# Kernel optimization log

Measured on AMD Instinct MI355X. Metric: run time of the kernel, lower is better.

The kernel has to match this reference:

```python
import jax, jax.numpy as jnp
import numpy as np

N = 100000
E = 1600000
IN_C, HID_C, OUT_C = 64, 64, 32


def setup_inputs() -> dict:
    key = jax.random.key(0)
    ks = jax.random.split(key, 8)
    x = jax.random.normal(ks[0], (N, IN_C), dtype=jnp.float32)
    edge_index = jax.random.randint(ks[1], (2, E), 0, N, dtype=jnp.int64)
    # GCNConv weights (glorot-ish scale) and biases
    W1 = jax.random.normal(ks[2], (IN_C, HID_C), dtype=jnp.float32) / np.sqrt(IN_C)
    b1 = jnp.zeros((HID_C,), dtype=jnp.float32)
    W2 = jax.random.normal(ks[3], (HID_C, HID_C), dtype=jnp.float32) / np.sqrt(HID_C)
    b2 = jnp.zeros((HID_C,), dtype=jnp.float32)
    Wlin = jax.random.normal(ks[4], (HID_C, OUT_C), dtype=jnp.float32) / np.sqrt(HID_C)
    blin = jnp.zeros((OUT_C,), dtype=jnp.float32)
    return {"x": x, "edge_index": edge_index, "W1": W1, "b1": b1,
            "W2": W2, "b2": b2, "Wlin": Wlin, "blin": blin}


def _gcn_norm(edge_index):
    # PyG GCNConv default: add self-loops, symmetric normalization.
    loop = jnp.arange(N, dtype=edge_index.dtype)
    row = jnp.concatenate([edge_index[0], loop])  # source nodes [E+N]
    col = jnp.concatenate([edge_index[1], loop])  # target nodes [E+N]
    deg = jax.ops.segment_sum(jnp.ones_like(col, dtype=jnp.float32), col,
                              num_segments=N)
    dinv = jnp.where(deg > 0, deg ** -0.5, 0.0)
    norm = dinv[row] * dinv[col]  # [E+N]
    return row, col, norm


def _gcn_conv(h, W, b, row, col, norm):
    h = h @ W                                  # [N, F_out]
    msg = h[row] * norm[:, None]               # gather + scale, [E+N, F_out]
    out = jax.ops.segment_sum(msg, col, num_segments=N)  # scatter-add
    return out + b


def reference(x, edge_index, W1, b1, W2, b2, Wlin, blin):
    row, col, norm = _gcn_norm(edge_index)
    h = jax.nn.relu(_gcn_conv(x, W1, b1, row, col, norm))
    h = jax.nn.relu(_gcn_conv(h, W2, b2, row, col, norm))
    return h @ Wlin + blin
```

## Files before the change

### kernel.cpp

```cpp
#include <hip/hip_runtime.h>
#include <hip/hip_fp16.h>

#define IN_C 64
#define HID_C 64
#define OUT_C 32
#define S_NODES  512
#define S_CAP  12288
#define CHUNK_E 4096

typedef _Float16 f16_t;
typedef f16_t f16x2 __attribute__((ext_vector_type(2)));

__device__ __forceinline__ float dot2(unsigned int a, unsigned int b, float c) {
#if __has_builtin(__builtin_amdgcn_fdot2)
    return __builtin_amdgcn_fdot2(*(f16x2*)&a, *(f16x2*)&b, c, false);
#else
    float2 af = __half22float2(*(__half2*)&a);
    float2 bf = __half22float2(*(__half2*)&b);
    return fmaf(af.x, bf.x, fmaf(af.y, bf.y, c));
#endif
}

__device__ __forceinline__ int wave_iscan(int x, int lane) {
#pragma unroll
    for (int o = 1; o < 64; o <<= 1) {
        int y = __shfl_up(x, o);
        if (lane >= o) x += y;
    }
    return x;
}

__global__ __launch_bounds__(256) void fat(const void* ei, int E,
                                           int* bcur, int NB,
                                           int* __restrict__ staging,
                                           int NEB, int GB,
                                           const float* __restrict__ x,
                                           const float* __restrict__ W1,
                                           float* __restrict__ t32, int n,
                                           const float* __restrict__ W2,
                                           const float* __restrict__ Wlin,
                                           unsigned short* __restrict__ Wh2,
                                           unsigned short* __restrict__ Whl) {
    __shared__ __align__(16) int smem[5128];
    int tid = threadIdx.x;
    int b = blockIdx.x;
    if (b < NEB) {
        int* cnt = smem;          int* boff = smem + 256;
        int* lcur = smem + 512;   int* gbase = smem + 768;
        int* stg = smem + 1024;
        int* ps64 = smem + 5120;
        int* wsum = smem + 5121;
        int lane = tid & 63, wv = tid >> 6;
        if (tid == 0) *ps64 = 1;
        cnt[tid] = 0;
        __syncthreads();
        if (2 * tid + 1 < 2 * E && ((const int*)ei)[2 * tid + 1] != 0) *ps64 = 0;
        __syncthreads();
        int is64 = *ps64;
        int e0 = b * CHUNK_E;
        int e1 = min(E, e0 + CHUNK_E);
        const int* ei32 = (const int*)ei;
        int rbuf[16];
        int bbuf[16];
        if (is64) {
#pragma unroll
            for (int k = 0; k < 16; k++) {
                int e = e0 + (k << 8) + tid;
                if (e < e1) {
                    int src = ei32[2 * e];
                    int dst = ei32[2 * (E + e)];
                    rbuf[k] = src | ((dst & 511) << 17);
                    int bk = dst >> 9;
                    bbuf[k] = bk;
                    atomicAdd(&cnt[bk], 1);
                } else bbuf[k] = -1;
            }
        } else {
#pragma unroll
            for (int k = 0; k < 16; k++) {
                int e = e0 + (k << 8) + tid;
                if (e < e1) {
                    int src = ei32[e];
                    int dst = ei32[E + e];
                    rbuf[k] = src | ((dst & 511) << 17);
                    int bk = dst >> 9;
                    bbuf[k] = bk;
                    atomicAdd(&cnt[bk], 1);
                } else bbuf[k] = -1;
            }
        }
        __syncthreads();
        int v = cnt[tid];
        int xx = wave_iscan(v, lane);
        if (lane == 63) wsum[wv] = xx;
        __syncthreads();
        int add = 0;
#pragma unroll
        for (int w = 0; w < 3; w++) add += (w < wv) ? wsum[w] : 0;
        int bo = xx + add - v;
        boff[tid] = bo;
        lcur[tid] = bo;
        __syncthreads();
#pragma unroll
        for (int k = 0; k < 16; k++) {
            if (bbuf[k] >= 0) {
                int p = atomicAdd(&lcur[bbuf[k]], 1);
                stg[p] = rbuf[k];
            }
        }
        __syncthreads();
        if (tid < NB && cnt[tid] > 0) gbase[tid] = atomicAdd(&bcur[tid], cnt[tid]);
        __syncthreads();
        int sw = tid >> 4, sl = tid & 15;
        for (int bk = sw; bk < NB; bk += 16) {
            int c = cnt[bk];
            if (c == 0) continue;
            int o = boff[bk], g = gbase[bk];
            size_t gb = (size_t)bk * S_CAP;
            for (int j = sl; j < c; j += 16) {
                if (g + j < S_CAP) staging[gb + g + j] = stg[o + j];
            }
        }
    } else if (b < NEB + GB) {
        uint4* sA = (uint4*)smem;
        int bb = b - NEB;
        int lane = tid & 63, wave = tid >> 6;
        unsigned int wu[32];
#pragma unroll
        for (int k = 0; k < 32; k++) {
            f16x2 p;
            p.x = (f16_t)W1[(2 * k) * 64 + lane];
            p.y = (f16_t)W1[(2 * k + 1) * 64 + lane];
            wu[k] = *(unsigned int*)&p;
        }
        int base = bb * 32;
        const float2* A2 = (const float2*)x;
        int lim = n * 32;
        for (int i = tid; i < 1024; i += 256) {
            int gi = base * 32 + i;
            float2 v = (gi < lim) ? A2[gi] : make_float2(0.f, 0.f);
            ((__half2*)sA)[i] = __floats2half2_rn(v.x, v.y);
        }
        __syncthreads();
        int r0 = base + wave * 8;
        int r1 = min(r0 + 8, n);
        for (int r = r0; r < r1; r++) {
            int rr = r - base;
            float a0 = 0.f, a1 = 0.f;
#pragma unroll
            for (int j = 0; j < 8; j++) {
                uint4 u = sA[rr * 8 + j];
                a0 = dot2(u.x, wu[4 * j], a0);
                a1 = dot2(u.y, wu[4 * j + 1], a1);
                a0 = dot2(u.z, wu[4 * j + 2], a0);
                a1 = dot2(u.w, wu[4 * j + 3], a1);
            }
            t32[(size_t)r * 64 + lane] = a0 + a1;
        }
    } else {
        for (int i = tid; i < 4096; i += 256) {
            int r = i >> 6, c = i & 63;
            f16_t h2 = (f16_t)W2[r * 64 + c];
            Wh2[c * 64 + r] = *(unsigned short*)&h2;
        }
        for (int i = tid; i < 2048; i += 256) {
            int r = i >> 5, c = i & 31;
            f16_t h = (f16_t)Wlin[r * 32 + c];
            Whl[c * 64 + r] = *(unsigned short*)&h;
        }
    }
}

__global__ __launch_bounds__(256) void place_fine(const int* __restrict__ staging,
                                                  const int* __restrict__ bcur,
                                                  int* __restrict__ offs,
                                                  float* __restrict__ dinv,
                                                  int* __restrict__ rec,
                                                  const float* __restrict__ t32,
                                                  unsigned short* __restrict__ t16,
                                                  int N, int NB) {
    __shared__ int sdeg[S_NODES];
    __shared__ int curs[S_NODES];
    __shared__ int sb[256];
    __shared__ float sdinv[S_NODES];
    __shared__ int wsum[4];
    int tid = threadIdx.x;
    int lane = tid & 63, wv = tid >> 6;
    int v = (tid < NB) ? min(bcur[tid], S_CAP) : 0;
    sdeg[tid] = 0;
    sdeg[tid + 256] = 0;
    int xx = wave_iscan(v, lane);
    if (lane == 63) wsum[wv] = xx;
    __syncthreads();
    int add = 0;
#pragma unroll
    for (int w = 0; w < 3; w++) add += (w < wv) ? wsum[w] : 0;
    sb[tid] = xx + add;
    __syncthreads();
    int cnt = min(bcur[blockIdx.x], S_CAP);
    int bbase = sb[blockIdx.x] - cnt;
    if (blockIdx.x == NB - 1 && tid == 0) offs[N] = sb[255];
    int base = blockIdx.x * S_NODES;
    int nn = min(S_NODES, N - base);
    size_t sbase = (size_t)blockIdx.x * S_CAP;
    for (int j = tid; j < cnt; j += 256) atomicAdd(&sdeg[staging[sbase + j] >> 17], 1);
    __syncthreads();
    int d0 = sdeg[2 * tid], d1 = sdeg[2 * tid + 1];
    int t = d0 + d1;
    int x2 = wave_iscan(t, lane);
    if (lane == 63) wsum[wv] = x2;
    __syncthreads();
    int add2 = 0;
#pragma unroll
    for (int w = 0; w < 3; w++) add2 += (w < wv) ? wsum[w] : 0;
    int pre = bbase + x2 + add2 - t;
    curs[2 * tid] = pre;
    curs[2 * tid + 1] = pre + d0;
    float dv0 = rsqrtf((float)(d0 + 1));
    float dv1 = rsqrtf((float)(d1 + 1));
    sdinv[2 * tid] = dv0;
    sdinv[2 * tid + 1] = dv1;
    if (2 * tid < nn) {
        offs[base + 2 * tid] = pre;
        dinv[base + 2 * tid] = dv0;
    }
    if (2 * tid + 1 < nn) {
        offs[base + 2 * tid + 1] = pre + d0;
        dinv[base + 2 * tid + 1] = dv1;
    }
    __syncthreads();
    for (int j = tid; j < cnt; j += 256) {
        int pk = staging[sbase + j];
        int p = atomicAdd(&curs[pk >> 17], 1);
        rec[p] = pk & 0x1FFFF;
    }
    const float4* tin = (const float4*)t32 + (size_t)base * 16;
    uint2* tout = (uint2*)t16 + (size_t)base * 16;
    int jmax = nn * 16;
    for (int j = tid; j < jmax; j += 256) {
        float4 vv = tin[j];
        float w = sdinv[j >> 4];
        __half2 h0 = __floats2half2_rn(vv.x * w, vv.y * w);
        __half2 h1 = __floats2half2_rn(vv.z * w, vv.w * w);
        tout[j] = make_uint2(*(unsigned int*)&h0, *(unsigned int*)&h1);
    }
}

__device__ __forceinline__ void agg_consume(const uint4& v, float w, float s[8]) {
    float2 f0 = __half22float2(*(__half2*)&v.x);
    float2 f1 = __half22float2(*(__half2*)&v.y);
    float2 f2 = __half22float2(*(__half2*)&v.z);
    float2 f3 = __half22float2(*(__half2*)&v.w);
    s[0] = fmaf(f0.x, w, s[0]);
    s[1] = fmaf(f0.y, w, s[1]);
    s[2] = fmaf(f1.x, w, s[2]);
    s[3] = fmaf(f1.y, w, s[3]);
    s[4] = fmaf(f2.x, w, s[4]);
    s[5] = fmaf(f2.y, w, s[5]);
    s[6] = fmaf(f3.x, w, s[6]);
    s[7] = fmaf(f3.y, w, s[7]);
}

template <int NU>
__device__ __forceinline__ void agg_chunk(const uint4* __restrict__ t4,
                                          const int* __restrict__ rec,
                                          int beg, int node, int m, int i,
                                          int g, int gl, float s[8]) {
    int srcs[NU];
    float ws[NU];
    uint4 vs[NU];
#pragma unroll
    for (int u = 0; u < NU; u++) {
        int it = i + u * 8 + g;
        srcs[u] = (it == 0) ? node : ((it < m) ? rec[beg + it - 1] : node);
        ws[u] = (it < m) ? 1.f : 0.f;
    }
#pragma unroll
    for (int u = 0; u < NU; u++) vs[u] = t4[(size_t)srcs[u] * 8 + gl];
#pragma unroll
    for (int u = 0; u < NU; u++) agg_consume(vs[u], ws[u], s);
}

__global__ void aggregate(const unsigned short* __restrict__ t,
                          const int* __restrict__ offs, const int* __restrict__ rec,
                          const float* __restrict__ dinv, const float* __restrict__ bias,
                          unsigned short* __restrict__ acc, int n) {
    int wave = (blockIdx.x * blockDim.x + threadIdx.x) >> 6;
    int lane = threadIdx.x & 63;
    if (wave >= n) return;
    int g = lane >> 3;
    int gl = lane & 7;
    int beg = offs[wave], end = offs[wave + 1];
    int m = end - beg + 1;
    const uint4* t4 = (const uint4*)t;
    float s[8] = {0.f, 0.f, 0.f, 0.f, 0.f, 0.f, 0.f, 0.f};
    int i = 0;
    for (; m - i > 24; i += 32) agg_chunk<4>(t4, rec, beg, wave, m, i, g, gl, s);
    int rem = m - i;
    if (rem > 16)     agg_chunk<3>(t4, rec, beg, wave, m, i, g, gl, s);
    else if (rem > 8) agg_chunk<2>(t4, rec, beg, wave, m, i, g, gl, s);
    else if (rem > 0) agg_chunk<1>(t4, rec, beg, wave, m, i, g, gl, s);
#pragma unroll
    for (int k = 0; k < 8; k++) {
        s[k] += __shfl_xor(s[k], 8);
        s[k] += __shfl_xor(s[k], 16);
        s[k] += __shfl_xor(s[k], 32);
    }
    if (g == 0) {
        float d = dinv[wave];
        const float4* b4 = (const float4*)bias;
        float4 bb0 = b4[gl * 2], bb1 = b4[gl * 2 + 1];
        float o0 = fmaxf(fmaf(s[0], d, bb0.x), 0.f);
        float o1 = fmaxf(fmaf(s[1], d, bb0.y), 0.f);
        float o2 = fmaxf(fmaf(s[2], d, bb0.z), 0.f);
        float o3 = fmaxf(fmaf(s[3], d, bb0.w), 0.f);
        float o4 = fmaxf(fmaf(s[4], d, bb1.x), 0.f);
        float o5 = fmaxf(fmaf(s[5], d, bb1.y), 0.f);
        float o6 = fmaxf(fmaf(s[6], d, bb1.z), 0.f);
        float o7 = fmaxf(fmaf(s[7], d, bb1.w), 0.f);
        __half2 p0 = __floats2half2_rn(o0, o1);
        __half2 p1 = __floats2half2_rn(o2, o3);
        __half2 p2 = __floats2half2_rn(o4, o5);
        __half2 p3 = __floats2half2_rn(o6, o7);
        ((uint4*)acc)[(size_t)wave * 8 + gl] =
            make_uint4(*(unsigned int*)&p0, *(unsigned int*)&p1,
                       *(unsigned int*)&p2, *(unsigned int*)&p3);
    }
}

__global__ __launch_bounds__(256) void gemm64(const unsigned short* __restrict__ in,
                                              const unsigned short* __restrict__ Wh,
                                              unsigned short* __restrict__ out,
                                              const float* __restrict__ dinv, int n) {
    __shared__ uint4 sA[32 * 8];
    int tid = threadIdx.x;
    int lane = tid & 63, wave = tid >> 6;
    unsigned int wu[32];
    {
        const uint4* col = (const uint4*)(Wh + (size_t)lane * 64);
#pragma unroll
        for (int j = 0; j < 8; j++) {
            uint4 w4 = col[j];
            wu[4 * j] = w4.x; wu[4 * j + 1] = w4.y;
            wu[4 * j + 2] = w4.z; wu[4 * j + 3] = w4.w;
        }
    }
    int base = blockIdx.x * 32;
    const uint2* A2 = (const uint2*)in;
    int lim = n * 16;
    for (int i = tid; i < 512; i += 256) {
        int gi = base * 16 + i;
        ((uint2*)sA)[i] = (gi < lim) ? A2[gi] : make_uint2(0u, 0u);
    }
    __syncthreads();
    int r0 = base + wave * 8;
    int r1 = min(r0 + 8, n);
    for (int r = r0; r < r1; r++) {
        int rr = r - base;
        float a0 = 0.f, a1 = 0.f;
#pragma unroll
        for (int j = 0; j < 8; j++) {
            uint4 u = sA[rr * 8 + j];
            a0 = dot2(u.x, wu[4 * j], a0);
            a1 = dot2(u.y, wu[4 * j + 1], a1);
            a0 = dot2(u.z, wu[4 * j + 2], a0);
            a1 = dot2(u.w, wu[4 * j + 3], a1);
        }
        __half hv = __float2half_rn((a0 + a1) * dinv[r]);
        out[(size_t)r * 64 + lane] = *(unsigned short*)&hv;
    }
}

__global__ __launch_bounds__(256) void gemm32(const unsigned short* __restrict__ in,
                                              const unsigned short* __restrict__ Wh,
                                              const float* __restrict__ b,
                                              float* __restrict__ out, int n) {
    __shared__ uint4 sA[32 * 8];
    int tid = threadIdx.x;
    int lane = tid & 63, wave = tid >> 6;
    int c = lane & 31;
    unsigned int wu[32];
    {
        const uint4* col = (const uint4*)(Wh + (size_t)c * 64);
#pragma unroll
        for (int j = 0; j < 8; j++) {
            uint4 w4 = col[j];
            wu[4 * j] = w4.x; wu[4 * j + 1] = w4.y;
            wu[4 * j + 2] = w4.z; wu[4 * j + 3] = w4.w;
        }
    }
    float bl = b[c];
    int base = blockIdx.x * 32;
    const uint2* A2 = (const uint2*)in;
    int lim = n * 16;
    for (int i = tid; i < 512; i += 256) {
        int gi = base * 16 + i;
        ((uint2*)sA)[i] = (gi < lim) ? A2[gi] : make_uint2(0u, 0u);
    }
    __syncthreads();
    int r0 = base + wave * 8;
    int r1 = min(r0 + 8, n);
    for (int r = r0; r < r1; r++) {
        int rr = r - base;
        float a0 = 0.f, a1 = 0.f;
#pragma unroll
        for (int j = 0; j < 8; j++) {
            uint4 u = sA[rr * 8 + j];
            a0 = dot2(u.x, wu[4 * j], a0);
            a1 = dot2(u.y, wu[4 * j + 1], a1);
            a0 = dot2(u.z, wu[4 * j + 2], a0);
            a1 = dot2(u.w, wu[4 * j + 3], a1);
        }
        if (lane < 32) out[(size_t)r * 32 + c] = bl + a0 + a1;
    }
}

extern "C" void kernel_launch(void* const* d_in, const int* in_sizes, int n_in,
                              void* d_out, int out_size, void* d_ws, size_t ws_size,
                              hipStream_t stream) {
    (void)n_in; (void)out_size; (void)ws_size;
    const float* x    = (const float*)d_in[0];
    const void*  ei   = d_in[1];
    const float* W1   = (const float*)d_in[2];
    const float* b1   = (const float*)d_in[3];
    const float* W2   = (const float*)d_in[4];
    const float* b2   = (const float*)d_in[5];
    const float* Wlin = (const float*)d_in[6];
    const float* blin = (const float*)d_in[7];
    float* out = (float*)d_out;

    const int N = in_sizes[0] / IN_C;
    const int E = in_sizes[1] / 2;
    const int NB = (N + S_NODES - 1) / S_NODES;
    const int NEB = (E + CHUNK_E - 1) / CHUNK_E;
    const int GB = (N + 31) / 32;

    char* ws = (char*)d_ws;
    size_t off = 0;
    auto alloc = [&](size_t bytes) -> void* {
        size_t a = (off + 255) & ~(size_t)255;
        off = a + bytes;
        return (void*)(ws + a);
    };
    int*   offs    = (int*)  alloc((size_t)(N + 1) * 4);
    float* dinv    = (float*)alloc((size_t)N * 4);
    int*   bcur    = (int*)  alloc((size_t)NB * 4);
    int*   rec     = (int*)  alloc((size_t)E * 4);
    int*   staging = (int*)  alloc((size_t)NB * S_CAP * 4);
    float* t32     = (float*)alloc((size_t)N * HID_C * 4);
    unsigned short* t16 = (unsigned short*)alloc((size_t)N * HID_C * 2);
    unsigned short* Wh2 = (unsigned short*)alloc(64 * 64 * 2);
    unsigned short* Whl = (unsigned short*)alloc(64 * 32 * 2);
    unsigned short* acc = (unsigned short*)t32;

    hipMemsetAsync(bcur, 0, (size_t)NB * 4, stream);

    fat<<<NEB + GB + 1, 256, 0, stream>>>(ei, E, bcur, NB, staging, NEB, GB,
                                          x, W1, t32, N, W2, Wlin, Wh2, Whl);
    place_fine<<<NB, 256, 0, stream>>>(staging, bcur, offs, dinv, rec,
                                       t32, t16, N, NB);

    aggregate<<<(N + 3) / 4, 256, 0, stream>>>(t16, offs, rec, dinv, b1, acc, N);
    gemm64<<<GB, 256, 0, stream>>>(acc, Wh2, t16, dinv, N);
    aggregate<<<(N + 3) / 4, 256, 0, stream>>>(t16, offs, rec, dinv, b2, acc, N);
    gemm32<<<GB, 256, 0, stream>>>(acc, Whl, blin, out, N);
}
```

Baseline: 259.3 us.

## Widen place_fine to 1024 threads and use fma_mix in aggregation

The place_fine kernel now runs 1024 threads per block instead of 256. Each thread handles one node for the degree scan, and the loops over staging entries and feature conversion are strided by 1024, which gives more parallelism per block because there are only NB blocks. Separately, the aggregation inner loop replaces the half-to-float conversion plus FMA with inline v_fma_mix_f32 assembly, which multiplies an fp16 half directly into an fp32 accumulator. The inline asm ties the code to the CDNA ISA and may limit compiler scheduling.

```diff
diff --git a/kernel.cpp b/kernel.cpp
--- a/kernel.cpp
+++ b/kernel.cpp
@@ -19,6 +19,13 @@
     float2 bf = __half22float2(*(__half2*)&b);
     return fmaf(af.x, bf.x, fmaf(af.y, bf.y, c));
 #endif
+}
+
+__device__ __forceinline__ void mix2(float& s0, float& s1, unsigned int p, float w) {
+    asm("v_fma_mix_f32 %0, %2, %3, %0 op_sel:[0,0,0] op_sel_hi:[1,0,0]\n\t"
+        "v_fma_mix_f32 %1, %2, %3, %1 op_sel:[1,0,0] op_sel_hi:[1,0,0]"
+        : "+v"(s0), "+v"(s1)
+        : "v"(p), "v"(w));
 }
 
 __device__ __forceinline__ int wave_iscan(int x, int lane) {
@@ -171,31 +178,35 @@
     }
 }
 
-__global__ __launch_bounds__(256) void place_fine(const int* __restrict__ staging,
-                                                  const int* __restrict__ bcur,
-                                                  int* __restrict__ offs,
-                                                  float* __restrict__ dinv,
-                                                  int* __restrict__ rec,
-                                                  const float* __restrict__ t32,
-                                                  unsigned short* __restrict__ t16,
-                                                  int N, int NB) {
+__global__ __launch_bounds__(1024) void place_fine(const int* __restrict__ staging,
+                                                   const int* __restrict__ bcur,
+                                                   int* __restrict__ offs,
+                                                   float* __restrict__ dinv,
+                                                   int* __restrict__ rec,
+                                                   const float* __restrict__ t32,
+                                                   unsigned short* __restrict__ t16,
+                                                   int N, int NB) {
     __shared__ int sdeg[S_NODES];
     __shared__ int curs[S_NODES];
     __shared__ int sb[256];
     __shared__ float sdinv[S_NODES];
-    __shared__ int wsum[4];
+    __shared__ int wsum[16];
     int tid = threadIdx.x;
     int lane = tid & 63, wv = tid >> 6;
-    int v = (tid < NB) ? min(bcur[tid], S_CAP) : 0;
-    sdeg[tid] = 0;
-    sdeg[tid + 256] = 0;
-    int xx = wave_iscan(v, lane);
-    if (lane == 63) wsum[wv] = xx;
-    __syncthreads();
-    int add = 0;
-#pragma unroll
-    for (int w = 0; w < 3; w++) add += (w < wv) ? wsum[w] : 0;
-    sb[tid] = xx + add;
+    if (tid < S_NODES) sdeg[tid] = 0;
+    if (tid < 256) {
+        int v = (tid < NB) ? min(bcur[tid], S_CAP) : 0;
+        int xx = wave_iscan(v, lane);
+        if (lane == 63) wsum[wv] = xx;
+        sb[tid] = xx;
+    }
+    __syncthreads();
+    if (tid < 256) {
+        int add = 0;
+#pragma unroll
+        for (int w = 0; w < 3; w++) add += (w < wv) ? wsum[w] : 0;
+        sb[tid] += add;
+    }
     __syncthreads();
     int cnt = min(bcur[blockIdx.x], S_CAP);
     int bbase = sb[blockIdx.x] - cnt;
@@ -203,33 +214,27 @@
     int base = blockIdx.x * S_NODES;
     int nn = min(S_NODES, N - base);
     size_t sbase = (size_t)blockIdx.x * S_CAP;
-    for (int j = tid; j < cnt; j += 256) atomicAdd(&sdeg[staging[sbase + j] >> 17], 1);
-    __syncthreads();
-    int d0 = sdeg[2 * tid], d1 = sdeg[2 * tid + 1];
-    int t = d0 + d1;
-    int x2 = wave_iscan(t, lane);
-    if (lane == 63) wsum[wv] = x2;
-    __syncthreads();
-    int add2 = 0;
-#pragma unroll
-    for (int w = 0; w < 3; w++) add2 += (w < wv) ? wsum[w] : 0;
-    int pre = bbase + x2 + add2 - t;
-    curs[2 * tid] = pre;
-    curs[2 * tid + 1] = pre + d0;
-    float dv0 = rsqrtf((float)(d0 + 1));
-    float dv1 = rsqrtf((float)(d1 + 1));
-    sdinv[2 * tid] = dv0;
-    sdinv[2 * tid + 1] = dv1;
-    if (2 * tid < nn) {
-        offs[base + 2 * tid] = pre;
-        dinv[base + 2 * tid] = dv0;
-    }
-    if (2 * tid + 1 < nn) {
-        offs[base + 2 * tid + 1] = pre + d0;
-        dinv[base + 2 * tid + 1] = dv1;
-    }
-    __syncthreads();
-    for (int j = tid; j < cnt; j += 256) {
+    for (int j = tid; j < cnt; j += 1024) atomicAdd(&sdeg[staging[sbase + j] >> 17], 1);
+    __syncthreads();
+    int d = (tid < S_NODES) ? sdeg[tid] : 0;
+    int x2 = wave_iscan(d, lane);
+    if (tid < S_NODES && lane == 63) wsum[wv] = x2;
+    __syncthreads();
+    if (tid < S_NODES) {
+        int add2 = 0;
+#pragma unroll
+        for (int w = 0; w < 7; w++) add2 += (w < wv) ? wsum[w] : 0;
+        int pre = bbase + x2 + add2 - d;
+        curs[tid] = pre;
+        float dv = rsqrtf((float)(d + 1));
+        sdinv[tid] = dv;
+        if (tid < nn) {
+            offs[base + tid] = pre;
+            dinv[base + tid] = dv;
+        }
+    }
+    __syncthreads();
+    for (int j = tid; j < cnt; j += 1024) {
         int pk = staging[sbase + j];
         int p = atomicAdd(&curs[pk >> 17], 1);
         rec[p] = pk & 0x1FFFF;
@@ -237,7 +242,7 @@
     const float4* tin = (const float4*)t32 + (size_t)base * 16;
     uint2* tout = (uint2*)t16 + (size_t)base * 16;
     int jmax = nn * 16;
-    for (int j = tid; j < jmax; j += 256) {
+    for (int j = tid; j < jmax; j += 1024) {
         float4 vv = tin[j];
         float w = sdinv[j >> 4];
         __half2 h0 = __floats2half2_rn(vv.x * w, vv.y * w);
@@ -247,18 +252,10 @@
 }
 
 __device__ __forceinline__ void agg_consume(const uint4& v, float w, float s[8]) {
-    float2 f0 = __half22float2(*(__half2*)&v.x);
-    float2 f1 = __half22float2(*(__half2*)&v.y);
-    float2 f2 = __half22float2(*(__half2*)&v.z);
-    float2 f3 = __half22float2(*(__half2*)&v.w);
-    s[0] = fmaf(f0.x, w, s[0]);
-    s[1] = fmaf(f0.y, w, s[1]);
-    s[2] = fmaf(f1.x, w, s[2]);
-    s[3] = fmaf(f1.y, w, s[3]);
-    s[4] = fmaf(f2.x, w, s[4]);
-    s[5] = fmaf(f2.y, w, s[5]);
-    s[6] = fmaf(f3.x, w, s[6]);
-    s[7] = fmaf(f3.y, w, s[7]);
+    mix2(s[0], s[1], v.x, w);
+    mix2(s[2], s[3], v.y, w);
+    mix2(s[4], s[5], v.z, w);
+    mix2(s[6], s[7], v.w, w);
 }
 
 template <int NU>
@@ -457,8 +454,8 @@
 
     fat<<<NEB + GB + 1, 256, 0, stream>>>(ei, E, bcur, NB, staging, NEB, GB,
                                           x, W1, t32, N, W2, Wlin, Wh2, Whl);
-    place_fine<<<NB, 256, 0, stream>>>(staging, bcur, offs, dinv, rec,
-                                       t32, t16, N, NB);
+    place_fine<<<NB, 1024, 0, stream>>>(staging, bcur, offs, dinv, rec,
+                                        t32, t16, N, NB);
 
     aggregate<<<(N + 3) / 4, 256, 0, stream>>>(t16, offs, rec, dinv, b1, acc, N);
     gemm64<<<GB, 256, 0, stream>>>(acc, Wh2, t16, dinv, N);
```

After: 245.3 us (median of 2 runs). -5.4%, faster.
